# Performance work log

Measured on AMD Instinct MI355X. Metric: run time of the kernel, lower is better.

The kernel has to match this reference:

```python
import jax, jax.numpy as jnp
import numpy as np

NUM_EXPERTS = 128
INPUT_DIM = 128
HIDDEN_DIM = 512
OUTPUT_DIM = 128
TOKENS_PER_EXPERT = 2048


def make_identity_experts(num_experts, input_dim, output_dim):
    # identical to the torch helper: zeros with ones on the (square) diagonal
    d = min(input_dim, output_dim)
    w = jnp.zeros((num_experts, input_dim, output_dim), dtype=jnp.float32)
    idx = jnp.arange(d)
    return w.at[:, idx, idx].set(1.0)


def setup_inputs() -> dict:
    key = jax.random.key(0)
    k_tok, = jax.random.split(key, 1)
    group_token = jax.random.normal(
        k_tok, (NUM_EXPERTS, TOKENS_PER_EXPERT, INPUT_DIM), dtype=jnp.float32)
    weights1 = make_identity_experts(NUM_EXPERTS, INPUT_DIM, HIDDEN_DIM)
    weights2 = make_identity_experts(NUM_EXPERTS, HIDDEN_DIM, OUTPUT_DIM)
    return {"group_token": group_token, "weights1": weights1, "weights2": weights2}


def reference(group_token, weights1, weights2):
    # grouped GEMM 1: per-expert [T, in] @ [in, hid]
    h = jnp.einsum('etd,edh->eth', group_token, weights1)
    # exact (erf-based) GELU, matching torch.nn.functional.gelu default
    h = jax.nn.gelu(h, approximate=False)
    # grouped GEMM 2: per-expert [T, hid] @ [hid, out]
    out = jnp.einsum('eth,eho->eto', h, weights2)
    return out
```

## Files before the change

### kernel.cpp

```cpp
#include <hip/hip_runtime.h>
#include <hip/hip_bf16.h>
#include <stdint.h>

typedef __attribute__((ext_vector_type(8))) short s8v;
typedef __attribute__((ext_vector_type(4))) float f4v;

#define NE   128
#define NT   2048
#define DIN  128
#define DH   512
#define DOUT 128

#define MFMA32(a,b,c) __builtin_amdgcn_mfma_f32_16x16x32_bf16(a,b,c,0,0,0)

#define GLOAD16(g,l) __builtin_amdgcn_global_load_lds( \
    (const __attribute__((address_space(1))) void*)(g), \
    (__attribute__((address_space(3))) void*)(l), 16, 0, 0)

#define WAIT_VM(N) asm volatile("s_waitcnt vmcnt(" #N ")" ::: "memory")
#define BAR() do { asm volatile("" ::: "memory"); \
                   __builtin_amdgcn_s_barrier();  \
                   asm volatile("" ::: "memory"); } while (0)

__device__ __forceinline__ __hip_bfloat162 pk2(float a, float b) {
  float2 t; t.x = a; t.y = b;
  return __float22bfloat162_rn(t);
}

__device__ __forceinline__ s8v pack8(float4 a, float4 b) {
  union { s8v v; __hip_bfloat162 h[4]; } u;
  u.h[0] = pk2(a.x, a.y); u.h[1] = pk2(a.z, a.w);
  u.h[2] = pk2(b.x, b.y); u.h[3] = pk2(b.z, b.w);
  return u.v;
}

__device__ __forceinline__ float gelu_f(float x) {
  float x2 = x * x;
  float p  = __builtin_fmaf(x2, 0.07135481f, 1.5957691f);
  float e  = __expf(-x * p);
  return x * __builtin_amdgcn_rcpf(1.0f + e);
}

__device__ __forceinline__ float4 gelu4(f4v v) {
  float4 r;
  r.x = gelu_f(v[0]); r.y = gelu_f(v[1]);
  r.z = gelu_f(v[2]); r.w = gelu_f(v[3]);
  return r;
}

__global__ __launch_bounds__(256) void pack_weights(
    const float* __restrict__ W1, const float* __restrict__ W2,
    ushort* __restrict__ W1F, ushort* __restrict__ W2F) {
  const int tid  = threadIdx.x;
  const int lane = tid & 63, w = tid >> 6;
  const int q    = lane >> 4, l16 = lane & 15;
  const int e    = blockIdx.x >> 4, s = blockIdx.x & 15;

  const float* W1e = W1 + (size_t)e * (DIN * DH);
  const float* W2e = W2 + (size_t)e * (DH * DOUT);

#pragma unroll
  for (int i = 0; i < 2; ++i) {
    const int g  = w + 4 * i;
    const int ht = 2 * s + (g >> 2);
    const int ks = g & 3;
    float v[8];
#pragma unroll
    for (int j = 0; j < 8; ++j)
      v[j] = W1e[(size_t)(ks * 32 + 8 * q + j) * DH + ht * 16 + l16];
    float4 a; a.x = v[0]; a.y = v[1]; a.z = v[2]; a.w = v[3];
    float4 b; b.x = v[4]; b.y = v[5]; b.z = v[6]; b.w = v[7];
    *(s8v*)(W1F + ((((size_t)e * 32 + ht) * 4) + ks) * 512 + lane * 8) = pack8(a, b);
  }

#pragma unroll
  for (int i = 0; i < 2; ++i) {
    const int ot = w + 4 * i;
    const int ct = s;
    float v[8];
#pragma unroll
    for (int j = 0; j < 8; ++j) {
      const int sig = (j < 4) ? (4 * q + j) : (16 + 4 * q + (j - 4));
      v[j] = W2e[(size_t)(ct * 32 + sig) * DOUT + ot * 16 + l16];
    }
    float4 a; a.x = v[0]; a.y = v[1]; a.z = v[2]; a.w = v[3];
    float4 b; b.x = v[4]; b.y = v[5]; b.z = v[6]; b.w = v[7];
    *(s8v*)(W2F + (((size_t)e * 16 + ct) * 8 + ot) * 512 + lane * 8) = pack8(a, b);
  }
}

__global__ __launch_bounds__(256, 3) void moe_fused(
    const float* __restrict__ X, const ushort* __restrict__ W1F,
    const ushort* __restrict__ W2F, float* __restrict__ Out) {
  __shared__ __align__(16) ushort W1s[2][4096];
  __shared__ __align__(16) ushort W2s[2][4096];

  const int tid  = threadIdx.x;
  const int lane = tid & 63;
  const int wid  = tid >> 6;
  const int q    = lane >> 4;
  const int l16  = lane & 15;

  const int bid  = blockIdx.x;
  const int wk   = ((bid & 7) << 8) | (bid >> 3);
  const int e    = wk >> 4;
  const int tile = wk & 15;

  const float* Xe  = X + ((size_t)e * NT + (size_t)tile * 128) * DIN;
  const ushort* W1e = W1F + (size_t)e * 65536;
  const ushort* W2e = W2F + (size_t)e * 65536;
  float* Oe = Out + ((size_t)e * NT + (size_t)tile * 128) * DOUT;

  s8v xf[2][4];
#pragma unroll
  for (int mt = 0; mt < 2; ++mt) {
#pragma unroll
    for (int ks = 0; ks < 4; ++ks) {
      const float* p = Xe + (size_t)(wid * 32 + mt * 16 + l16) * DIN + ks * 32 + q * 8;
      float4 v0 = *(const float4*)p;
      float4 v1 = *(const float4*)(p + 4);
      xf[mt][ks] = pack8(v0, v1);
    }
  }

  const f4v zero4 = {0.0f, 0.0f, 0.0f, 0.0f};
  f4v oacc[2][8];
#pragma unroll
  for (int mt = 0; mt < 2; ++mt)
#pragma unroll
    for (int ot = 0; ot < 8; ++ot) oacc[mt][ot] = zero4;

  auto stage = [&](int chunk, int b) {
    const ushort* g1 = W1e + chunk * 4096;
    const ushort* g2 = W2e + chunk * 4096;
#pragma unroll
    for (int i = 0; i < 2; ++i) {
      int u = i * 256 + tid;
      GLOAD16(g1 + u * 8, &W1s[b][u * 8]);
      GLOAD16(g2 + u * 8, &W2s[b][u * 8]);
    }
  };

  asm volatile("" ::: "memory");

  stage(0, 0);

  for (int c = 0; c < 16; ++c) {
    const int buf = c & 1;
    WAIT_VM(0);
    BAR();
    if (c < 15) stage(c + 1, buf ^ 1);

    f4v h0[2]; h0[0] = zero4; h0[1] = zero4;
#pragma unroll
    for (int kp = 0; kp < 2; ++kp) {
      s8v af0 = *(const s8v*)&W1s[buf][(kp * 2 + 0) * 512 + lane * 8];
      s8v af1 = *(const s8v*)&W1s[buf][(kp * 2 + 1) * 512 + lane * 8];
      __builtin_amdgcn_s_setprio(1);
      h0[0] = MFMA32(af0, xf[0][kp * 2 + 0], h0[0]);
      h0[1] = MFMA32(af0, xf[1][kp * 2 + 0], h0[1]);
      h0[0] = MFMA32(af1, xf[0][kp * 2 + 1], h0[0]);
      h0[1] = MFMA32(af1, xf[1][kp * 2 + 1], h0[1]);
      __builtin_amdgcn_s_setprio(0);
    }
    float4 ga0 = gelu4(h0[0]);
    float4 ga1 = gelu4(h0[1]);

    f4v h1[2]; h1[0] = zero4; h1[1] = zero4;
#pragma unroll
    for (int kp = 0; kp < 2; ++kp) {
      s8v af0 = *(const s8v*)&W1s[buf][(4 + kp * 2 + 0) * 512 + lane * 8];
      s8v af1 = *(const s8v*)&W1s[buf][(4 + kp * 2 + 1) * 512 + lane * 8];
      __builtin_amdgcn_s_setprio(1);
      h1[0] = MFMA32(af0, xf[0][kp * 2 + 0], h1[0]);
      h1[1] = MFMA32(af0, xf[1][kp * 2 + 0], h1[1]);
      h1[0] = MFMA32(af1, xf[0][kp * 2 + 1], h1[0]);
      h1[1] = MFMA32(af1, xf[1][kp * 2 + 1], h1[1]);
      __builtin_amdgcn_s_setprio(0);
    }

    s8v a8_0 = pack8(ga0, gelu4(h1[0]));
    s8v a8_1 = pack8(ga1, gelu4(h1[1]));

#pragma unroll
    for (int op = 0; op < 4; ++op) {
      s8v b0 = *(const s8v*)&W2s[buf][(op * 2 + 0) * 512 + lane * 8];
      s8v b1 = *(const s8v*)&W2s[buf][(op * 2 + 1) * 512 + lane * 8];
      __builtin_amdgcn_s_setprio(1);
      oacc[0][op * 2 + 0] = MFMA32(a8_0, b0, oacc[0][op * 2 + 0]);
      oacc[1][op * 2 + 0] = MFMA32(a8_1, b0, oacc[1][op * 2 + 0]);
      oacc[0][op * 2 + 1] = MFMA32(a8_0, b1, oacc[0][op * 2 + 1]);
      oacc[1][op * 2 + 1] = MFMA32(a8_1, b1, oacc[1][op * 2 + 1]);
      __builtin_amdgcn_s_setprio(0);
    }
  }

#pragma unroll
  for (int mt = 0; mt < 2; ++mt) {
    const int mb = wid * 32 + mt * 16 + 4 * q;
#pragma unroll
    for (int ot = 0; ot < 8; ++ot) {
      float* p = Oe + (size_t)mb * DOUT + ot * 16 + l16;
      p[0 * DOUT] = oacc[mt][ot][0];
      p[1 * DOUT] = oacc[mt][ot][1];
      p[2 * DOUT] = oacc[mt][ot][2];
      p[3 * DOUT] = oacc[mt][ot][3];
    }
  }
}

extern "C" void kernel_launch(void* const* d_in, const int* in_sizes, int n_in,
                              void* d_out, int out_size, void* d_ws, size_t ws_size,
                              hipStream_t stream) {
  const float* X  = (const float*)d_in[0];
  const float* W1 = (const float*)d_in[1];
  const float* W2 = (const float*)d_in[2];
  float* Out = (float*)d_out;

  ushort* W1F = (ushort*)d_ws;
  ushort* W2F = (ushort*)d_ws + (size_t)NE * 65536;

  pack_weights<<<NE * 16, 256, 0, stream>>>(W1, W2, W1F, W2F);
  moe_fused<<<NE * (NT / 128), 256, 0, stream>>>(X, W1F, W2F, Out);
}
```

Baseline: 342.8 us.

## Fuse weight packing into main kernel with register-staged fp32 gathers

Removes the separate pack_weights launch and its bf16 workspace round trip. Each block now gathers fp32 weights from global memory into registers one chunk ahead, converts them to bf16 in the MFMA fragment layout, and writes them into the LDS double buffer after the current chunk's compute. This saves a kernel launch and the packed-weight write and read, but every one of the 2048 blocks now re-reads and re-converts its expert's fp32 weights with strided scalar loads. It also adds register pressure at 3 blocks per CU.

```diff
diff --git a/kernel.cpp b/kernel.cpp
--- a/kernel.cpp
+++ b/kernel.cpp
@@ -13,11 +13,7 @@
 
 #define MFMA32(a,b,c) __builtin_amdgcn_mfma_f32_16x16x32_bf16(a,b,c,0,0,0)
 
-#define GLOAD16(g,l) __builtin_amdgcn_global_load_lds( \
-    (const __attribute__((address_space(1))) void*)(g), \
-    (__attribute__((address_space(3))) void*)(l), 16, 0, 0)
-
-#define WAIT_VM(N) asm volatile("s_waitcnt vmcnt(" #N ")" ::: "memory")
+#define LGKM0() asm volatile("s_waitcnt lgkmcnt(0)" ::: "memory")
 #define BAR() do { asm volatile("" ::: "memory"); \
                    __builtin_amdgcn_s_barrier();  \
                    asm volatile("" ::: "memory"); } while (0)
@@ -48,50 +44,9 @@
   return r;
 }
 
-__global__ __launch_bounds__(256) void pack_weights(
-    const float* __restrict__ W1, const float* __restrict__ W2,
-    ushort* __restrict__ W1F, ushort* __restrict__ W2F) {
-  const int tid  = threadIdx.x;
-  const int lane = tid & 63, w = tid >> 6;
-  const int q    = lane >> 4, l16 = lane & 15;
-  const int e    = blockIdx.x >> 4, s = blockIdx.x & 15;
-
-  const float* W1e = W1 + (size_t)e * (DIN * DH);
-  const float* W2e = W2 + (size_t)e * (DH * DOUT);
-
-#pragma unroll
-  for (int i = 0; i < 2; ++i) {
-    const int g  = w + 4 * i;
-    const int ht = 2 * s + (g >> 2);
-    const int ks = g & 3;
-    float v[8];
-#pragma unroll
-    for (int j = 0; j < 8; ++j)
-      v[j] = W1e[(size_t)(ks * 32 + 8 * q + j) * DH + ht * 16 + l16];
-    float4 a; a.x = v[0]; a.y = v[1]; a.z = v[2]; a.w = v[3];
-    float4 b; b.x = v[4]; b.y = v[5]; b.z = v[6]; b.w = v[7];
-    *(s8v*)(W1F + ((((size_t)e * 32 + ht) * 4) + ks) * 512 + lane * 8) = pack8(a, b);
-  }
-
-#pragma unroll
-  for (int i = 0; i < 2; ++i) {
-    const int ot = w + 4 * i;
-    const int ct = s;
-    float v[8];
-#pragma unroll
-    for (int j = 0; j < 8; ++j) {
-      const int sig = (j < 4) ? (4 * q + j) : (16 + 4 * q + (j - 4));
-      v[j] = W2e[(size_t)(ct * 32 + sig) * DOUT + ot * 16 + l16];
-    }
-    float4 a; a.x = v[0]; a.y = v[1]; a.z = v[2]; a.w = v[3];
-    float4 b; b.x = v[4]; b.y = v[5]; b.z = v[6]; b.w = v[7];
-    *(s8v*)(W2F + (((size_t)e * 16 + ct) * 8 + ot) * 512 + lane * 8) = pack8(a, b);
-  }
-}
-
 __global__ __launch_bounds__(256, 3) void moe_fused(
-    const float* __restrict__ X, const ushort* __restrict__ W1F,
-    const ushort* __restrict__ W2F, float* __restrict__ Out) {
+    const float* __restrict__ X, const float* __restrict__ W1,
+    const float* __restrict__ W2, float* __restrict__ Out) {
   __shared__ __align__(16) ushort W1s[2][4096];
   __shared__ __align__(16) ushort W2s[2][4096];
 
@@ -106,10 +61,45 @@
   const int e    = wk >> 4;
   const int tile = wk & 15;
 
-  const float* Xe  = X + ((size_t)e * NT + (size_t)tile * 128) * DIN;
-  const ushort* W1e = W1F + (size_t)e * 65536;
-  const ushort* W2e = W2F + (size_t)e * 65536;
+  const float* Xe = X + ((size_t)e * NT + (size_t)tile * 128) * DIN;
   float* Oe = Out + ((size_t)e * NT + (size_t)tile * 128) * DOUT;
+
+  const float* w1p = W1 + (size_t)e * (DIN * DH)
+                   + (size_t)(wid * 32 + 8 * q) * DH + l16;
+  const float* w2p = W2 + (size_t)e * (DH * DOUT)
+                   + (size_t)(4 * q) * DOUT + wid * 16 + l16;
+
+  float ga[16], gb[16];
+  auto gather = [&]() {
+#pragma unroll
+    for (int j = 0; j < 8; ++j) {
+      ga[j]     = w1p[(size_t)j * DH];
+      ga[8 + j] = w1p[(size_t)j * DH + 16];
+    }
+#pragma unroll
+    for (int j = 0; j < 8; ++j) {
+      const int row = (j < 4) ? j : (12 + j);
+      gb[j]     = w2p[(size_t)row * DOUT];
+      gb[8 + j] = w2p[(size_t)row * DOUT + 64];
+    }
+    w1p += 32;
+    w2p += (size_t)32 * DOUT;
+  };
+
+  auto cvtwrite = [&](int b) {
+    float4 a0 = make_float4(ga[0],  ga[1],  ga[2],  ga[3]);
+    float4 a1 = make_float4(ga[4],  ga[5],  ga[6],  ga[7]);
+    float4 a2 = make_float4(ga[8],  ga[9],  ga[10], ga[11]);
+    float4 a3 = make_float4(ga[12], ga[13], ga[14], ga[15]);
+    *(s8v*)&W1s[b][(size_t)wid * 512 + lane * 8]       = pack8(a0, a1);
+    *(s8v*)&W1s[b][(size_t)(4 + wid) * 512 + lane * 8] = pack8(a2, a3);
+    float4 b0 = make_float4(gb[0],  gb[1],  gb[2],  gb[3]);
+    float4 b1 = make_float4(gb[4],  gb[5],  gb[6],  gb[7]);
+    float4 b2 = make_float4(gb[8],  gb[9],  gb[10], gb[11]);
+    float4 b3 = make_float4(gb[12], gb[13], gb[14], gb[15]);
+    *(s8v*)&W2s[b][(size_t)wid * 512 + lane * 8]       = pack8(b0, b1);
+    *(s8v*)&W2s[b][(size_t)(4 + wid) * 512 + lane * 8] = pack8(b2, b3);
+  };
 
   s8v xf[2][4];
 #pragma unroll
@@ -130,26 +120,13 @@
 #pragma unroll
     for (int ot = 0; ot < 8; ++ot) oacc[mt][ot] = zero4;
 
-  auto stage = [&](int chunk, int b) {
-    const ushort* g1 = W1e + chunk * 4096;
-    const ushort* g2 = W2e + chunk * 4096;
-#pragma unroll
-    for (int i = 0; i < 2; ++i) {
-      int u = i * 256 + tid;
-      GLOAD16(g1 + u * 8, &W1s[b][u * 8]);
-      GLOAD16(g2 + u * 8, &W2s[b][u * 8]);
-    }
-  };
-
-  asm volatile("" ::: "memory");
-
-  stage(0, 0);
+  gather();
+  cvtwrite(0);
+  gather();
+  LGKM0(); BAR();
 
   for (int c = 0; c < 16; ++c) {
     const int buf = c & 1;
-    WAIT_VM(0);
-    BAR();
-    if (c < 15) stage(c + 1, buf ^ 1);
 
     f4v h0[2]; h0[0] = zero4; h0[1] = zero4;
 #pragma unroll
@@ -193,6 +170,10 @@
       oacc[1][op * 2 + 1] = MFMA32(a8_1, b1, oacc[1][op * 2 + 1]);
       __builtin_amdgcn_s_setprio(0);
     }
+
+    if (c < 15) cvtwrite(buf ^ 1);
+    if (c < 14) gather();
+    if (c < 15) { LGKM0(); BAR(); }
   }
 
 #pragma unroll
@@ -216,10 +197,7 @@
   const float* W1 = (const float*)d_in[1];
   const float* W2 = (const float*)d_in[2];
   float* Out = (float*)d_out;
-
-  ushort* W1F = (ushort*)d_ws;
-  ushort* W2F = (ushort*)d_ws + (size_t)NE * 65536;
-
-  pack_weights<<<NE * 16, 256, 0, stream>>>(W1, W2, W1F, W2F);
-  moe_fused<<<NE * (NT / 128), 256, 0, stream>>>(X, W1F, W2F, Out);
-}
+  (void)d_ws; (void)ws_size;
+
+  moe_fused<<<NE * (NT / 128), 256, 0, stream>>>(X, W1, W2, Out);
+}
```

Measured after the change: 359.5 us. 1.05x slower.
